# Kernel optimization log

Measured on AMD Instinct MI355X. Metric: run time of the kernel, lower is better.

## Reference

```python
import jax, jax.numpy as jnp
import numpy as np

# Static config (matches init_kwargs / chosen geometry)
DIM, HEADS, WS, SHIFT = 96, 3, 7, 3
H, W = 56, 56
B = 64
N = WS * WS
HID = int(DIM * 4.0)
EPS = 1e-5


def _rel_tables():
    # relative_coords_table: (1, 2*WS-1, 2*WS-1, 2), log-spaced coords in [-1,1]
    c = np.arange(-(WS - 1), WS, dtype=np.float32)
    tab = np.stack(np.meshgrid(c, c, indexing='ij'), axis=-1)[None]
    tab = tab / (WS - 1) * 8.0
    tab = np.sign(tab) * np.log2(np.abs(tab) + 1.0) / np.log2(8.0)
    # relative_position_index: (N, N) int
    coords = np.stack(np.meshgrid(np.arange(WS), np.arange(WS), indexing='ij'))
    cf = coords.reshape(2, -1)
    rel = (cf[:, :, None] - cf[:, None, :]).transpose(1, 2, 0).astype(np.int64)
    rel[..., 0] += WS - 1
    rel[..., 1] += WS - 1
    rel[..., 0] *= 2 * WS - 1
    return jnp.asarray(tab), jnp.asarray(rel.sum(-1))

_TABLE, _RPI = _rel_tables()


def _shift_mask():
    # standard SW-MSA mask: (num_windows, N, N), 0 / -100
    img = np.zeros((1, H, W, 1), dtype=np.float32)
    cnt = 0
    segs = (slice(0, -WS), slice(-WS, -SHIFT), slice(-SHIFT, None))
    for hs in segs:
        for ws_ in segs:
            img[:, hs, ws_, :] = cnt
            cnt += 1
    mw = img.reshape(1, H // WS, WS, W // WS, WS, 1).transpose(0, 1, 3, 2, 4, 5).reshape(-1, N)
    am = mw[:, None, :] - mw[:, :, None]
    return jnp.asarray(np.where(am != 0, -100.0, 0.0).astype(np.float32))


def _ln(x, g, b):
    mu = x.mean(-1, keepdims=True)
    var = x.var(-1, keepdims=True)
    return (x - mu) * jax.lax.rsqrt(var + EPS) * g + b


def setup_inputs() -> dict:
    key = jax.random.key(0)
    ks = jax.random.split(key, 8)
    s = 0.02
    return {
        'x': jax.random.normal(ks[0], (B, H * W, DIM), jnp.float32),
        'attn_mask': _shift_mask(),
        'qkv_w': jax.random.normal(ks[1], (3 * DIM, DIM), jnp.float32) * s,
        'q_bias': jnp.zeros((DIM,), jnp.float32),
        'v_bias': jnp.zeros((DIM,), jnp.float32),
        'logit_scale': jnp.full((HEADS, 1, 1), np.log(10.0), jnp.float32),
        'cpb_w1': jax.random.normal(ks[2], (512, 2), jnp.float32) * s,
        'cpb_b1': jnp.zeros((512,), jnp.float32),
        'cpb_w2': jax.random.normal(ks[3], (HEADS, 512), jnp.float32) * s,
        'proj_w': jax.random.normal(ks[4], (DIM, DIM), jnp.float32) * s,
        'proj_b': jnp.zeros((DIM,), jnp.float32),
        'norm1_g': jnp.ones((DIM,), jnp.float32),
        'norm1_b': jnp.zeros((DIM,), jnp.float32),
        'fc1_w': jax.random.normal(ks[5], (HID, DIM), jnp.float32) * s,
        'fc1_b': jnp.zeros((HID,), jnp.float32),
        'fc2_w': jax.random.normal(ks[6], (DIM, HID), jnp.float32) * s,
        'fc2_b': jnp.zeros((DIM,), jnp.float32),
        'norm2_g': jnp.ones((DIM,), jnp.float32),
        'norm2_b': jnp.zeros((DIM,), jnp.float32),
    }


def reference(x, attn_mask, qkv_w, q_bias, v_bias, logit_scale, cpb_w1, cpb_b1,
              cpb_w2, proj_w, proj_b, norm1_g, norm1_b, fc1_w, fc1_b, fc2_w,
              fc2_b, norm2_g, norm2_b):
    Bx, L, C = x.shape
    d = C // HEADS
    nH, nWd = H // WS, W // WS
    shortcut = x

    xi = x.reshape(Bx, H, W, C)
    xi = jnp.roll(xi, (-SHIFT, -SHIFT), axis=(1, 2))
    # window partition -> (Bx*nH*nWd, N, C)
    xw = xi.reshape(Bx, nH, WS, nWd, WS, C).transpose(0, 1, 3, 2, 4, 5).reshape(-1, N, C)

    # qkv with q/v bias only (k bias fixed to zero)
    qkv_bias = jnp.concatenate([q_bias, jnp.zeros_like(v_bias), v_bias])
    qkv = (xw @ qkv_w.T + qkv_bias).reshape(-1, N, 3, HEADS, d).transpose(2, 0, 3, 1, 4)
    q, k, v = qkv[0], qkv[1], qkv[2]  # (B_, h, N, d)

    # cosine attention with clamped learnable temperature
    qn = q / jnp.maximum(jnp.linalg.norm(q, axis=-1, keepdims=True), 1e-12)
    kn = k / jnp.maximum(jnp.linalg.norm(k, axis=-1, keepdims=True), 1e-12)
    attn = jnp.einsum('bhnd,bhmd->bhnm', qn, kn)
    scale = jnp.exp(jnp.minimum(logit_scale, jnp.log(jnp.float32(100.0))))
    attn = attn * scale

    # continuous relative position bias via cpb_mlp
    tab = jax.nn.gelu(_TABLE @ cpb_w1.T + cpb_b1, approximate=False) @ cpb_w2.T
    tab = tab.reshape(-1, HEADS)
    rpb = tab[_RPI.reshape(-1)].reshape(N, N, HEADS).transpose(2, 0, 1)
    attn = attn + (16.0 * jax.nn.sigmoid(rpb))[None]

    # shift mask
    nWin = attn_mask.shape[0]
    attn = attn.reshape(-1, nWin, HEADS, N, N) + attn_mask[None, :, None]
    attn = jax.nn.softmax(attn.reshape(-1, HEADS, N, N), axis=-1)

    out = jnp.einsum('bhnm,bhmd->bnhd', attn, v).reshape(-1, N, C)
    out = out @ proj_w.T + proj_b

    # window reverse + un-shift
    out = out.reshape(Bx, nH, nWd, WS, WS, C).transpose(0, 1, 3, 2, 4, 5).reshape(Bx, H, W, C)
    out = jnp.roll(out, (SHIFT, SHIFT), axis=(1, 2)).reshape(Bx, L, C)

    # SwinV2 post-norm residuals
    x1 = shortcut + _ln(out, norm1_g, norm1_b)
    h = jax.nn.gelu(x1 @ fc1_w.T + fc1_b, approximate=False) @ fc2_w.T + fc2_b
    return x1 + _ln(h, norm2_g, norm2_b)
```

## Files before the change

kernel.cpp:

```cpp
#include <hip/hip_runtime.h>
#include <math.h>

#define BATCH 64
#define HW 56
#define CDIM 96
#define NHEADS 3
#define WSZ 7
#define NTOK 49
#define SHIFT_ 3
#define NWIN_TOT 4096
#define HID 384
#define NTOKENS (BATCH * HW * HW)
#define LN100 4.6051702f

typedef __attribute__((ext_vector_type(8))) short bf16x8;
typedef __attribute__((ext_vector_type(8))) _Float16 f16x8;
typedef __attribute__((ext_vector_type(4))) float f32x4;

__device__ inline f32x4 mfma16(bf16x8 a, bf16x8 b, f32x4 c) {
  return __builtin_amdgcn_mfma_f32_16x16x32_bf16(a, b, c, 0, 0, 0);
}
__device__ inline f32x4 mfma16h(f16x8 a, f16x8 b, f32x4 c) {
  return __builtin_amdgcn_mfma_f32_16x16x32_f16(a, b, c, 0, 0, 0);
}

__device__ inline unsigned short f2b(float f) {
  unsigned u = __float_as_uint(f);
  unsigned r = (u + 0x7FFFu + ((u >> 16) & 1u)) >> 16;
  return (unsigned short)r;
}
__device__ inline float blo(unsigned u) { return __uint_as_float(u << 16); }
__device__ inline float bhi(unsigned u) { return __uint_as_float(u & 0xFFFF0000u); }
__device__ inline unsigned packb(float a, float b) {
  return (unsigned)f2b(a) | ((unsigned)f2b(b) << 16);
}
__device__ inline unsigned packh(float a, float b) {
  _Float16 ha = (_Float16)a, hb = (_Float16)b;
  unsigned short ua = *(unsigned short*)&ha, ub = *(unsigned short*)&hb;
  return (unsigned)ua | ((unsigned)ub << 16);
}
__device__ inline float gelu_f(float v) {
  float a = fabsf(v) * 0.70710678118654752f;
  float t = 1.0f / fmaf(a, 0.3275911f, 1.0f);
  float p = t * fmaf(t, fmaf(t, fmaf(t, fmaf(t, 1.061405429f, -1.453152027f),
                                     1.421413741f), -0.284496736f), 0.254829592f);
  float er = 1.0f - p * __expf(-a * a);
  er = (v < 0.f) ? -er : er;
  return 0.5f * v * (1.0f + er);
}

__global__ __launch_bounds__(256) void wconv2_kernel(
    const float* __restrict__ qkv_w, const float* __restrict__ fc1_w,
    const float* __restrict__ fc2_w, const float* __restrict__ proj_w,
    unsigned* __restrict__ qkvf, unsigned* __restrict__ w1f,
    unsigned* __restrict__ w2f, unsigned* __restrict__ pwf) {
  int T = blockIdx.x * 256 + threadIdx.x;
  if (T < 3456) {
    int tk = T >> 6, l = T & 63;
    int n = tk / 3, ks = tk - n * 3;
    int o = n * 16 + (l & 15);
    const float* src = qkv_w + o * 96 + ks * 32 + (l >> 4) * 8;
    uint4 d;
    d.x = packb(src[0], src[1]); d.y = packb(src[2], src[3]);
    d.z = packb(src[4], src[5]); d.w = packb(src[6], src[7]);
    *(uint4*)&qkvf[(size_t)(tk * 64 + l) * 4] = d;
    return;
  }
  T -= 3456;
  if (T < 4608) {
    int tk = T >> 6, l = T & 63;
    int n = tk / 3, ks = tk - n * 3;
    int o = n * 16 + (l & 15);
    const float* src = fc1_w + o * 96 + ks * 32 + (l >> 4) * 8;
    uint4 d;
    d.x = packb(src[0], src[1]); d.y = packb(src[2], src[3]);
    d.z = packb(src[4], src[5]); d.w = packb(src[6], src[7]);
    *(uint4*)&w1f[(size_t)(tk * 64 + l) * 4] = d;
    return;
  }
  T -= 4608;
  if (T < 4608) {
    int tk = T >> 6, l = T & 63;
    int n = tk / 12, ks = tk - n * 12;
    int o = n * 16 + (l & 15);
    const float* src = fc2_w + o * 384 + ks * 32 + (l >> 4) * 8;
    uint4 d;
    d.x = packb(src[0], src[1]); d.y = packb(src[2], src[3]);
    d.z = packb(src[4], src[5]); d.w = packb(src[6], src[7]);
    *(uint4*)&w2f[(size_t)(tk * 64 + l) * 4] = d;
    return;
  }
  T -= 4608;
  if (T < 1152) {
    int tk = T >> 6, l = T & 63;
    int n = tk / 3, ks = tk - n * 3;
    int o = n * 16 + (l & 15);
    const float* src = proj_w + o * 96 + ks * 32 + (l >> 4) * 8;
    uint4 d;
    d.x = packb(src[0], src[1]); d.y = packb(src[2], src[3]);
    d.z = packb(src[4], src[5]); d.w = packb(src[6], src[7]);
    *(uint4*)&pwf[(size_t)(tk * 64 + l) * 4] = d;
  }
}

__global__ __launch_bounds__(512) void cpb_table_kernel(
    const float* __restrict__ w1, const float* __restrict__ b1,
    const float* __restrict__ w2, float* __restrict__ tabout) {
  int tid = threadIdx.x;
  if (tid >= 169 * 3) return;
  int e = tid / 3, h = tid - e * 3;
  int i = e / 13, j = e - i * 13;
  float ti = (float)(i - 6) * (8.0f / 6.0f);
  float tj = (float)(j - 6) * (8.0f / 6.0f);
  float sx = (ti > 0.f) ? 1.f : (ti < 0.f ? -1.f : 0.f);
  float sy = (tj > 0.f) ? 1.f : (tj < 0.f ? -1.f : 0.f);
  float tx = sx * log2f(fabsf(ti) + 1.f) * (1.0f / 3.0f);
  float ty = sy * log2f(fabsf(tj) + 1.f) * (1.0f / 3.0f);
  float acc = 0.f;
  for (int jj = 0; jj < 512; ++jj) {
    float hv = tx * w1[jj * 2 + 0] + ty * w1[jj * 2 + 1] + b1[jj];
    float g = 0.5f * hv * (1.f + erff(hv * 0.70710678118654752f));
    acc += g * w2[h * 512 + jj];
  }
  tabout[e * 3 + h] = acc;
}

__global__ __launch_bounds__(256) void bm_kernel(
    const float* __restrict__ tabout, const float* __restrict__ mask,
    float* __restrict__ bmtab) {
  int idx = blockIdx.x * 256 + threadIdx.x;
  if (idx >= 64 * NHEADS * NTOK * NTOK) return;
  int wi = idx / (NHEADS * 2401);
  int rem = idx - wi * (NHEADS * 2401);
  int h = rem / 2401, ij = rem - h * 2401;
  int i = ij / NTOK, j = ij - i * NTOK;
  int ri = (i / WSZ) - (j / WSZ) + 6;
  int ci = (i % WSZ) - (j % WSZ) + 6;
  int e = ri * 13 + ci;
  float v = tabout[e * 3 + h];
  bmtab[idx] = 16.f / (1.f + expf(-v)) + mask[(size_t)wi * 2401 + ij];
}

__global__ __launch_bounds__(256) void qkv_mfma_kernel(
    const float* __restrict__ x, const unsigned* __restrict__ qkvf,
    const float* __restrict__ q_bias, const float* __restrict__ v_bias,
    const float* __restrict__ logit_scale,
    unsigned* __restrict__ qws, unsigned* __restrict__ kws,
    unsigned* __restrict__ vws) {
  __shared__ unsigned xa[64 * 52];
  int tid = threadIdx.x, lane = tid & 63, wv = tid >> 6;
  size_t tok0 = (size_t)blockIdx.x * 64;

  for (int idx = tid; idx < 3072; idx += 256) {
    int t = idx / 48, c2 = idx - t * 48;
    const float2 s = *(const float2*)(x + (tok0 + t) * 96 + c2 * 2);
    xa[t * 52 + c2] = packb(s.x, s.y);
  }
  __syncthreads();

  int c15 = lane & 15, q4 = lane >> 4;
  bf16x8 afr[3];
  #pragma unroll
  for (int k = 0; k < 3; ++k)
    afr[k] = *(const bf16x8*)&xa[(wv * 16 + c15) * 52 + k * 16 + q4 * 4];

  f32x4 acc[18];
  #pragma unroll
  for (int n = 0; n < 18; ++n) acc[n] = f32x4{0.f, 0.f, 0.f, 0.f};
  #pragma unroll
  for (int n = 0; n < 18; ++n) {
    #pragma unroll
    for (int k = 0; k < 3; ++k) {
      bf16x8 b = *(const bf16x8*)&qkvf[(size_t)((n * 3 + k) * 64 + lane) * 4];
      acc[n] = mfma16(afr[k], b, acc[n]);
    }
  }

  int tokr0 = (int)tok0 + wv * 16 + q4 * 4;
  int wbase[4];
  #pragma unroll
  for (int i = 0; i < 4; ++i) {
    int tk = tokr0 + i;
    int bb = tk / 3136, rem = tk - bb * 3136;
    int R = rem / 56, C = rem - R * 56;
    int rr = R + 53; if (rr >= 56) rr -= 56;
    int cc = C + 53; if (cc >= 56) cc -= 56;
    int wr = rr / 7, tr2 = rr - wr * 7;
    int wc = cc / 7, tc2 = cc - wc * 7;
    wbase[i] = (bb * 64 + wr * 8 + wc) * 2352 + (tr2 * 7 + tc2) * 16;
  }

  #pragma unroll
  for (int h = 0; h < 3; ++h) {
    float sc = expf(fminf(logit_scale[h], LN100));
    {
      f32x4 a0 = acc[2 * h], a1 = acc[2 * h + 1];
      float b0 = q_bias[h * 32 + c15], b1 = q_bias[h * 32 + 16 + c15];
      unsigned pk[8];
      #pragma unroll
      for (int i = 0; i < 4; ++i) {
        float va = a0[i] + b0, vb = a1[i] + b1;
        float ss = va * va + vb * vb;
        ss += __shfl_xor(ss, 1, 64); ss += __shfl_xor(ss, 2, 64);
        ss += __shfl_xor(ss, 4, 64); ss += __shfl_xor(ss, 8, 64);
        float inv = sc / fmaxf(sqrtf(ss), 1e-12f);
        va *= inv; vb *= inv;
        float pa = __shfl_xor(va, 1, 64), pb = __shfl_xor(vb, 1, 64);
        pk[i] = packb(va, pa); pk[4 + i] = packb(vb, pb);
      }
      if (!(lane & 1)) {
        int dw0 = c15 >> 1;
        #pragma unroll
        for (int i = 0; i < 4; ++i) {
          size_t base = (size_t)wbase[i] + h * 784;
          qws[base + dw0] = pk[i];
          qws[base + 8 + dw0] = pk[4 + i];
        }
      }
    }
    {
      f32x4 a0 = acc[6 + 2 * h], a1 = acc[7 + 2 * h];
      unsigned pk[8];
      #pragma unroll
      for (int i = 0; i < 4; ++i) {
        float va = a0[i], vb = a1[i];
        float ss = va * va + vb * vb;
        ss += __shfl_xor(ss, 1, 64); ss += __shfl_xor(ss, 2, 64);
        ss += __shfl_xor(ss, 4, 64); ss += __shfl_xor(ss, 8, 64);
        float inv = 1.f / fmaxf(sqrtf(ss), 1e-12f);
        va *= inv; vb *= inv;
        float pa = __shfl_xor(va, 1, 64), pb = __shfl_xor(vb, 1, 64);
        pk[i] = packb(va, pa); pk[4 + i] = packb(vb, pb);
      }
      if (!(lane & 1)) {
        int dw0 = c15 >> 1;
        #pragma unroll
        for (int i = 0; i < 4; ++i) {
          size_t base = (size_t)wbase[i] + h * 784;
          kws[base + dw0] = pk[i];
          kws[base + 8 + dw0] = pk[4 + i];
        }
      }
    }
    {
      f32x4 a0 = acc[12 + 2 * h], a1 = acc[13 + 2 * h];
      float b0 = v_bias[h * 32 + c15], b1 = v_bias[h * 32 + 16 + c15];
      unsigned pk[8];
      #pragma unroll
      for (int i = 0; i < 4; ++i) {
        float va = a0[i] + b0, vb = a1[i] + b1;
        float pa = __shfl_xor(va, 1, 64), pb = __shfl_xor(vb, 1, 64);
        pk[i] = packb(va, pa); pk[4 + i] = packb(vb, pb);
      }
      if (!(lane & 1)) {
        int dw0 = c15 >> 1;
        #pragma unroll
        for (int i = 0; i < 4; ++i) {
          size_t base = (size_t)wbase[i] + h * 784;
          vws[base + dw0] = pk[i];
          vws[base + 8 + dw0] = pk[4 + i];
        }
      }
    }
  }
}

__global__ __launch_bounds__(256) void attn_fused_kernel(
    const unsigned* __restrict__ qws, const unsigned* __restrict__ kws,
    const unsigned* __restrict__ vws, const float* __restrict__ bmtab,
    const unsigned* __restrict__ pwf, const float* __restrict__ proj_b,
    const float* __restrict__ x, const float* __restrict__ n1g,
    const float* __restrict__ n1b, float* __restrict__ out) {
  __shared__ __align__(16) unsigned smem[10368];
  _Float16* VtS  = (_Float16*)smem;
  unsigned* obuf = (unsigned*)smem;
  _Float16* Ph   = (_Float16*)((char*)smem + 13824);
  unsigned* Phd  = (unsigned*)((char*)smem + 13824);
  float*    ybuf = (float*)((char*)smem + 13824);

  int tid = threadIdx.x, lane = tid & 63, wv = tid >> 6;
  int c15 = lane & 15, q4 = lane >> 4;
  int win = blockIdx.x;
  int b = win >> 6, wi = win & 63, wh = wi >> 3, wcx = wi & 7;
  size_t wroot = (size_t)win * 2352;

  for (int idx = tid; idx < 768; idx += 256) {
    int h2 = idx >> 8, rem = idx & 255;
    int t = rem >> 2, dg = rem & 3;
    int tc2 = t > 48 ? 48 : t;
    uint4 v4 = *(const uint4*)&vws[wroot + h2 * 784 + tc2 * 16 + dg * 4];
    _Float16* dst = &VtS[h2 * 2304 + (dg * 8) * 72 + t];
    dst[0 * 72] = (_Float16)blo(v4.x); dst[1 * 72] = (_Float16)bhi(v4.x);
    dst[2 * 72] = (_Float16)blo(v4.y); dst[3 * 72] = (_Float16)bhi(v4.y);
    dst[4 * 72] = (_Float16)blo(v4.z); dst[5 * 72] = (_Float16)bhi(v4.z);
    dst[6 * 72] = (_Float16)blo(v4.w); dst[7 * 72] = (_Float16)bhi(v4.w);
  }
  __syncthreads();

  f32x4 oall[3][2];
  #pragma unroll
  for (int t = 0; t < 3; ++t)
    #pragma unroll
    for (int n2 = 0; n2 < 2; ++n2) oall[t][n2] = f32x4{0.f, 0.f, 0.f, 0.f};

  #pragma unroll
  for (int t = 0; t < 3; ++t) {
    int id = wv * 3 + t;
    int h = id >> 2, mm = id & 3;
    size_t wb = wroot + (size_t)h * 784;

    int tq = mm * 16 + c15; if (tq > 48) tq = 48;
    bf16x8 qf = *(const bf16x8*)&qws[wb + tq * 16 + q4 * 4];
    bf16x8 kf[4];
    #pragma unroll
    for (int n = 0; n < 4; ++n) {
      int tk = n * 16 + c15; if (tk > 48) tk = 48;
      kf[n] = *(const bf16x8*)&kws[wb + tk * 16 + q4 * 4];
    }

    f32x4 s[4];
    #pragma unroll
    for (int n = 0; n < 4; ++n)
      s[n] = mfma16(qf, kf[n], f32x4{0.f, 0.f, 0.f, 0.f});

    const float* bm = bmtab + ((size_t)wi * 3 + h) * 2401;
    #pragma unroll
    for (int i = 0; i < 4; ++i) {
      int rw = mm * 16 + 4 * q4 + i;
      if (rw < 49) {
        const float* br = bm + rw * 49;
        #pragma unroll
        for (int n = 0; n < 4; ++n) {
          int j = n * 16 + c15;
          s[n][i] = (j < 49) ? (s[n][i] + br[j]) : -1e30f;
        }
      } else {
        #pragma unroll
        for (int n = 0; n < 4; ++n)
          if (n * 16 + c15 >= 49) s[n][i] = -1e30f;
      }
    }

    #pragma unroll
    for (int i = 0; i < 4; ++i) {
      float mx = fmaxf(fmaxf(s[0][i], s[1][i]), fmaxf(s[2][i], s[3][i]));
      mx = fmaxf(mx, __shfl_xor(mx, 1, 64)); mx = fmaxf(mx, __shfl_xor(mx, 2, 64));
      mx = fmaxf(mx, __shfl_xor(mx, 4, 64)); mx = fmaxf(mx, __shfl_xor(mx, 8, 64));
      float sum = 0.f;
      #pragma unroll
      for (int n = 0; n < 4; ++n) { float e = __expf(s[n][i] - mx); s[n][i] = e; sum += e; }
      sum += __shfl_xor(sum, 1, 64); sum += __shfl_xor(sum, 2, 64);
      sum += __shfl_xor(sum, 4, 64); sum += __shfl_xor(sum, 8, 64);
      float inv = 1.f / sum;
      #pragma unroll
      for (int n = 0; n < 4; ++n) s[n][i] *= inv;
    }

    #pragma unroll
    for (int n = 0; n < 4; ++n)
      #pragma unroll
      for (int i = 0; i < 4; ++i) {
        float pv = s[n][i];
        float pn = __shfl_xor(pv, 1, 64);
        if (!(lane & 1)) {
          int row = mm * 16 + 4 * q4 + i;
          Phd[h * 2304 + row * 36 + n * 8 + (c15 >> 1)] = packh(pv, pn);
        }
      }
    asm volatile("s_waitcnt lgkmcnt(0)" ::: "memory");
    __builtin_amdgcn_sched_barrier(0);

    #pragma unroll
    for (int ks = 0; ks < 2; ++ks) {
      f16x8 pa = *(const f16x8*)&Ph[h * 4608 + (mm * 16 + c15) * 72 + ks * 32 + q4 * 8];
      #pragma unroll
      for (int n2 = 0; n2 < 2; ++n2) {
        f16x8 vb = *(const f16x8*)&VtS[h * 2304 + (n2 * 16 + c15) * 72 + ks * 32 + q4 * 8];
        oall[t][n2] = mfma16h(pa, vb, oall[t][n2]);
      }
    }
  }
  __syncthreads();

  #pragma unroll
  for (int t = 0; t < 3; ++t) {
    int id = wv * 3 + t;
    int h = id >> 2, mm = id & 3;
    #pragma unroll
    for (int n2 = 0; n2 < 2; ++n2)
      #pragma unroll
      for (int i = 0; i < 4; ++i) {
        float ov = oall[t][n2][i];
        float on = __shfl_xor(ov, 1, 64);
        if (!(lane & 1))
          obuf[(mm * 16 + 4 * q4 + i) * 52 + h * 16 + n2 * 8 + (c15 >> 1)] = packb(ov, on);
      }
  }
  __syncthreads();

  bf16x8 oa[3];
  #pragma unroll
  for (int ks = 0; ks < 3; ++ks)
    oa[ks] = *(const bf16x8*)&obuf[(wv * 16 + c15) * 52 + ks * 16 + q4 * 4];
  f32x4 pr[6];
  #pragma unroll
  for (int n = 0; n < 6; ++n) pr[n] = f32x4{0.f, 0.f, 0.f, 0.f};
  #pragma unroll
  for (int n = 0; n < 6; ++n)
    #pragma unroll
    for (int ks = 0; ks < 3; ++ks) {
      bf16x8 bfr = *(const bf16x8*)&pwf[(size_t)((n * 3 + ks) * 64 + lane) * 4];
      pr[n] = mfma16(oa[ks], bfr, pr[n]);
    }

  #pragma unroll
  for (int n = 0; n < 6; ++n) {
    int col = n * 16 + c15;
    float bo = proj_b[col];
    #pragma unroll
    for (int i = 0; i < 4; ++i)
      ybuf[(wv * 16 + 4 * q4 + i) * 100 + col] = pr[n][i] + bo;
  }
  __syncthreads();

  int t = tid >> 2, pp = tid & 3;
  if (t < 49) {
    const float* yrow = ybuf + t * 100 + pp * 24;
    float s1 = 0.f;
    #pragma unroll
    for (int c = 0; c < 24; ++c) s1 += yrow[c];
    s1 += __shfl_xor(s1, 1, 64); s1 += __shfl_xor(s1, 2, 64);
    float mu = s1 * (1.f / 96.f);
    float v2 = 0.f;
    #pragma unroll
    for (int c = 0; c < 24; ++c) { float d = yrow[c] - mu; v2 += d * d; }
    v2 += __shfl_xor(v2, 1, 64); v2 += __shfl_xor(v2, 2, 64);
    float rs = rsqrtf(v2 * (1.f / 96.f) + 1e-5f);
    int tr = (t * 9363) >> 16, tc = t - tr * 7;
    int R = wh * 7 + tr + SHIFT_; if (R >= HW) R -= HW;
    int C = wcx * 7 + tc + SHIFT_; if (C >= HW) C -= HW;
    size_t base = ((size_t)(b * 3136 + R * 56 + C)) * 96 + pp * 24;
    #pragma unroll
    for (int c4 = 0; c4 < 6; ++c4) {
      float4 xv = *(const float4*)(x + base + c4 * 4);
      float4 gv = *(const float4*)(n1g + pp * 24 + c4 * 4);
      float4 bv = *(const float4*)(n1b + pp * 24 + c4 * 4);
      float4 ov;
      ov.x = xv.x + (yrow[c4 * 4 + 0] - mu) * rs * gv.x + bv.x;
      ov.y = xv.y + (yrow[c4 * 4 + 1] - mu) * rs * gv.y + bv.y;
      ov.z = xv.z + (yrow[c4 * 4 + 2] - mu) * rs * gv.z + bv.z;
      ov.w = xv.w + (yrow[c4 * 4 + 3] - mu) * rs * gv.w + bv.w;
      *(float4*)(out + base + c4 * 4) = ov;
    }
  }
}

__global__ __launch_bounds__(256) void mlp_mfma_kernel(
    const unsigned* __restrict__ w1f, const float* __restrict__ fc1_b,
    const unsigned* __restrict__ w2f, const float* __restrict__ fc2_b,
    const float* __restrict__ n2g, const float* __restrict__ n2b,
    float* __restrict__ xio) {
  __shared__ unsigned xa[64 * 52];
  __shared__ unsigned hid[64 * 196];
  __shared__ float mu_s[64], rs_s[64];
  int tid = threadIdx.x, lane = tid & 63, wv = tid >> 6;
  int c15 = lane & 15, q4 = lane >> 4;
  size_t tok0 = (size_t)blockIdx.x * 64;

  for (int idx = tid; idx < 3072; idx += 256) {
    int t = idx / 48, c2 = idx - t * 48;
    const float2 s = *(const float2*)(xio + (tok0 + t) * 96 + c2 * 2);
    xa[t * 52 + c2] = packb(s.x, s.y);
  }
  __syncthreads();

  bf16x8 afr[4][3];
  #pragma unroll
  for (int m = 0; m < 4; ++m)
    #pragma unroll
    for (int k = 0; k < 3; ++k)
      afr[m][k] = *(const bf16x8*)&xa[(m * 16 + c15) * 52 + k * 16 + q4 * 4];
  f32x4 acc[4][6];
  #pragma unroll
  for (int m = 0; m < 4; ++m)
    #pragma unroll
    for (int n = 0; n < 6; ++n) acc[m][n] = f32x4{0.f, 0.f, 0.f, 0.f};
  #pragma unroll
  for (int n = 0; n < 6; ++n) {
    #pragma unroll
    for (int k = 0; k < 3; ++k) {
      bf16x8 b = *(const bf16x8*)&w1f[(size_t)(((6 * wv + n) * 3 + k) * 64 + lane) * 4];
      #pragma unroll
      for (int m = 0; m < 4; ++m) acc[m][n] = mfma16(afr[m][k], b, acc[m][n]);
    }
  }
  unsigned short* hidb = (unsigned short*)hid;
  #pragma unroll
  for (int n = 0; n < 6; ++n) {
    int col = (6 * wv + n) * 16 + c15;
    float bo = fc1_b[col];
    #pragma unroll
    for (int m = 0; m < 4; ++m) {
      #pragma unroll
      for (int i = 0; i < 4; ++i) {
        float g = gelu_f(acc[m][n][i] + bo);
        hidb[(m * 16 + q4 * 4 + i) * 392 + col] = f2b(g);
      }
    }
  }
  __syncthreads();

  f32x4 acc2[6];
  #pragma unroll
  for (int n = 0; n < 6; ++n) acc2[n] = f32x4{0.f, 0.f, 0.f, 0.f};
  #pragma unroll
  for (int k = 0; k < 12; ++k) {
    bf16x8 a = *(const bf16x8*)&hid[(wv * 16 + c15) * 196 + k * 16 + q4 * 4];
    #pragma unroll
    for (int n = 0; n < 6; ++n) {
      bf16x8 b = *(const bf16x8*)&w2f[(size_t)((n * 12 + k) * 64 + lane) * 4];
      acc2[n] = mfma16(a, b, acc2[n]);
    }
  }
  __syncthreads();

  float* ybuf = (float*)hid;
  #pragma unroll
  for (int n = 0; n < 6; ++n) {
    int col = n * 16 + c15;
    float bo = fc2_b[col];
    #pragma unroll
    for (int i = 0; i < 4; ++i)
      ybuf[(wv * 16 + q4 * 4 + i) * 100 + col] = acc2[n][i] + bo;
  }
  __syncthreads();

  {
    int t = tid >> 2, p = tid & 3;
    const float* row = ybuf + t * 100 + p * 24;
    float s = 0.f, s2 = 0.f;
    for (int c = 0; c < 24; ++c) { float v = row[c]; s += v; s2 += v * v; }
    s += __shfl_xor(s, 1, 64); s2 += __shfl_xor(s2, 1, 64);
    s += __shfl_xor(s, 2, 64); s2 += __shfl_xor(s2, 2, 64);
    if (p == 0) {
      float mu = s * (1.f / 96.f);
      float var = s2 * (1.f / 96.f) - mu * mu;
      mu_s[t] = mu;
      rs_s[t] = rsqrtf(fmaxf(var, 0.f) + 1e-5f);
    }
  }
  __syncthreads();

  for (int idx = tid; idx < 1536; idx += 256) {
    int t = idx / 24, c4 = (idx - t * 24) * 4;
    float mu = mu_s[t], rs = rs_s[t];
    float4 y4 = *(float4*)&ybuf[t * 100 + c4];
    float4 g4 = *(const float4*)&n2g[c4];
    float4 b4 = *(const float4*)&n2b[c4];
    float* gp = &xio[tok0 * 96 + t * 96 + c4];
    float4 x4 = *(const float4*)gp;
    float4 ov;
    ov.x = x4.x + (y4.x - mu) * rs * g4.x + b4.x;
    ov.y = x4.y + (y4.y - mu) * rs * g4.y + b4.y;
    ov.z = x4.z + (y4.z - mu) * rs * g4.z + b4.z;
    ov.w = x4.w + (y4.w - mu) * rs * g4.w + b4.w;
    *(float4*)gp = ov;
  }
}

extern "C" void kernel_launch(void* const* d_in, const int* in_sizes, int n_in,
                              void* d_out, int out_size, void* d_ws, size_t ws_size,
                              hipStream_t stream) {
  const float* x           = (const float*)d_in[0];
  const float* attn_mask   = (const float*)d_in[1];
  const float* qkv_w       = (const float*)d_in[2];
  const float* q_bias      = (const float*)d_in[3];
  const float* v_bias      = (const float*)d_in[4];
  const float* logit_scale = (const float*)d_in[5];
  const float* cpb_w1      = (const float*)d_in[6];
  const float* cpb_b1      = (const float*)d_in[7];
  const float* cpb_w2      = (const float*)d_in[8];
  const float* proj_w      = (const float*)d_in[9];
  const float* proj_b      = (const float*)d_in[10];
  const float* n1g         = (const float*)d_in[11];
  const float* n1b         = (const float*)d_in[12];
  const float* fc1_w       = (const float*)d_in[13];
  const float* fc1_b       = (const float*)d_in[14];
  const float* fc2_w       = (const float*)d_in[15];
  const float* fc2_b       = (const float*)d_in[16];
  const float* n2g         = (const float*)d_in[17];
  const float* n2b         = (const float*)d_in[18];
  float* out = (float*)d_out;

  float* tab     = (float*)d_ws;
  float* bmtab   = tab + 512;
  unsigned* qkvf = (unsigned*)(bmtab + 460992);
  unsigned* w1f  = qkvf + 13824;
  unsigned* w2f  = w1f + 18432;
  unsigned* pwf  = w2f + 18432;
  unsigned* qws  = pwf + 4608;
  unsigned* kws  = qws + 9633792;
  unsigned* vws  = kws + 9633792;

  wconv2_kernel<<<54, 256, 0, stream>>>(qkv_w, fc1_w, fc2_w, proj_w,
                                        qkvf, w1f, w2f, pwf);
  cpb_table_kernel<<<1, 512, 0, stream>>>(cpb_w1, cpb_b1, cpb_w2, tab);
  bm_kernel<<<(64 * NHEADS * NTOK * NTOK + 255) / 256, 256, 0, stream>>>(
      tab, attn_mask, bmtab);
  qkv_mfma_kernel<<<NTOKENS / 64, 256, 0, stream>>>(x, qkvf, q_bias, v_bias,
                                                    logit_scale, qws, kws, vws);
  attn_fused_kernel<<<NWIN_TOT, 256, 0, stream>>>(qws, kws, vws, bmtab,
                                                  pwf, proj_b, x, n1g, n1b, out);
  mlp_mfma_kernel<<<NTOKENS / 64, 256, 0, stream>>>(w1f, fc1_b, w2f, fc2_b,
                                                    n2g, n2b, out);
}
```

Baseline: 438.7 us.

## Emit bf16 copy of x1 from attention kernel and feed MLP directly

The attention epilogue now also writes a packed bf16 copy of the residual output x1 to a new workspace buffer. The MLP kernel loads its A fragments straight from that buffer in global memory, so the fp32 read, the conversion, the LDS staging and one barrier all go away. The hidden-layer store is also changed to pack two bf16 values per 32-bit write using a lane shuffle. This adds an extra write of about 38MB of bf16 in the attention kernel and needs more workspace. The fp32 x1 is still read later for the residual.

```diff
diff --git a/kernel.cpp b/kernel.cpp
--- a/kernel.cpp
+++ b/kernel.cpp
@@ -270,7 +270,8 @@
     const unsigned* __restrict__ vws, const float* __restrict__ bmtab,
     const unsigned* __restrict__ pwf, const float* __restrict__ proj_b,
     const float* __restrict__ x, const float* __restrict__ n1g,
-    const float* __restrict__ n1b, float* __restrict__ out) {
+    const float* __restrict__ n1b, float* __restrict__ out,
+    unsigned* __restrict__ x1bf) {
   __shared__ __align__(16) unsigned smem[10368];
   _Float16* VtS  = (_Float16*)smem;
   unsigned* obuf = (unsigned*)smem;
@@ -439,7 +440,9 @@
     int tr = (t * 9363) >> 16, tc = t - tr * 7;
     int R = wh * 7 + tr + SHIFT_; if (R >= HW) R -= HW;
     int C = wcx * 7 + tc + SHIFT_; if (C >= HW) C -= HW;
-    size_t base = ((size_t)(b * 3136 + R * 56 + C)) * 96 + pp * 24;
+    size_t tokorig = (size_t)(b * 3136 + R * 56 + C);
+    size_t base = tokorig * 96 + pp * 24;
+    unsigned bpk[12];
     #pragma unroll
     for (int c4 = 0; c4 < 6; ++c4) {
       float4 xv = *(const float4*)(x + base + c4 * 4);
@@ -451,7 +454,13 @@
       ov.z = xv.z + (yrow[c4 * 4 + 2] - mu) * rs * gv.z + bv.z;
       ov.w = xv.w + (yrow[c4 * 4 + 3] - mu) * rs * gv.w + bv.w;
       *(float4*)(out + base + c4 * 4) = ov;
-    }
+      bpk[c4 * 2 + 0] = packb(ov.x, ov.y);
+      bpk[c4 * 2 + 1] = packb(ov.z, ov.w);
+    }
+    unsigned* xb = x1bf + tokorig * 48 + pp * 12;
+    *(uint4*)&xb[0] = *(uint4*)&bpk[0];
+    *(uint4*)&xb[4] = *(uint4*)&bpk[4];
+    *(uint4*)&xb[8] = *(uint4*)&bpk[8];
   }
 }
 
@@ -459,27 +468,20 @@
     const unsigned* __restrict__ w1f, const float* __restrict__ fc1_b,
     const unsigned* __restrict__ w2f, const float* __restrict__ fc2_b,
     const float* __restrict__ n2g, const float* __restrict__ n2b,
-    float* __restrict__ xio) {
-  __shared__ unsigned xa[64 * 52];
+    const unsigned* __restrict__ x1bf, float* __restrict__ xio) {
   __shared__ unsigned hid[64 * 196];
   __shared__ float mu_s[64], rs_s[64];
   int tid = threadIdx.x, lane = tid & 63, wv = tid >> 6;
   int c15 = lane & 15, q4 = lane >> 4;
   size_t tok0 = (size_t)blockIdx.x * 64;
 
-  for (int idx = tid; idx < 3072; idx += 256) {
-    int t = idx / 48, c2 = idx - t * 48;
-    const float2 s = *(const float2*)(xio + (tok0 + t) * 96 + c2 * 2);
-    xa[t * 52 + c2] = packb(s.x, s.y);
-  }
-  __syncthreads();
-
   bf16x8 afr[4][3];
   #pragma unroll
   for (int m = 0; m < 4; ++m)
     #pragma unroll
     for (int k = 0; k < 3; ++k)
-      afr[m][k] = *(const bf16x8*)&xa[(m * 16 + c15) * 52 + k * 16 + q4 * 4];
+      afr[m][k] = *(const bf16x8*)&x1bf[(tok0 + m * 16 + c15) * 48 + k * 16 + q4 * 4];
+
   f32x4 acc[4][6];
   #pragma unroll
   for (int m = 0; m < 4; ++m)
@@ -494,7 +496,6 @@
       for (int m = 0; m < 4; ++m) acc[m][n] = mfma16(afr[m][k], b, acc[m][n]);
     }
   }
-  unsigned short* hidb = (unsigned short*)hid;
   #pragma unroll
   for (int n = 0; n < 6; ++n) {
     int col = (6 * wv + n) * 16 + c15;
@@ -504,7 +505,11 @@
       #pragma unroll
       for (int i = 0; i < 4; ++i) {
         float g = gelu_f(acc[m][n][i] + bo);
-        hidb[(m * 16 + q4 * 4 + i) * 392 + col] = f2b(g);
+        float gn = __shfl_xor(g, 1, 64);
+        if (!(lane & 1)) {
+          int row = m * 16 + q4 * 4 + i;
+          hid[row * 196 + (6 * wv + n) * 8 + (c15 >> 1)] = packb(g, gn);
+        }
       }
     }
   }
@@ -601,6 +606,7 @@
   unsigned* qws  = pwf + 4608;
   unsigned* kws  = qws + 9633792;
   unsigned* vws  = kws + 9633792;
+  unsigned* x1bf = vws + 9633792;
 
   wconv2_kernel<<<54, 256, 0, stream>>>(qkv_w, fc1_w, fc2_w, proj_w,
                                         qkvf, w1f, w2f, pwf);
@@ -610,7 +616,8 @@
   qkv_mfma_kernel<<<NTOKENS / 64, 256, 0, stream>>>(x, qkvf, q_bias, v_bias,
                                                     logit_scale, qws, kws, vws);
   attn_fused_kernel<<<NWIN_TOT, 256, 0, stream>>>(qws, kws, vws, bmtab,
-                                                  pwf, proj_b, x, n1g, n1b, out);
+                                                  pwf, proj_b, x, n1g, n1b, out,
+                                                  x1bf);
   mlp_mfma_kernel<<<NTOKENS / 64, 256, 0, stream>>>(w1f, fc1_b, w2f, fc2_b,
-                                                    n2g, n2b, out);
-}
+                                                    n2g, n2b, x1bf, out);
+}
```

After: 531.8 us. +21.2%, slower.

## Fuse MLP into attention kernel per window, keeping x1 in shared memory

Applied to the files above, without the earlier changes.

Merges the MLP kernel into the windowed attention kernel. Each block now holds its window's 49 post-attention tokens (x1) in shared memory and runs fc1, GELU, fc2 and LayerNorm2 on them directly. This removes the global write and re-read of the intermediate activation tensor and one kernel launch. In exchange the block's shared memory grows to about 76KB, which may lower occupancy, and the MLP now processes 49-token tiles padded to 64, wasting MFMA work on the padding rows.

```diff
diff --git a/kernel.cpp b/kernel.cpp
--- a/kernel.cpp
+++ b/kernel.cpp
@@ -38,6 +38,11 @@
   _Float16 ha = (_Float16)a, hb = (_Float16)b;
   unsigned short ua = *(unsigned short*)&ha, ub = *(unsigned short*)&hb;
   return (unsigned)ua | ((unsigned)ub << 16);
+}
+__device__ inline bf16x8 mk8(unsigned d0, unsigned d1, unsigned d2, unsigned d3) {
+  union { unsigned u[4]; bf16x8 v; } c;
+  c.u[0] = d0; c.u[1] = d1; c.u[2] = d2; c.u[3] = d3;
+  return c.v;
 }
 __device__ inline float gelu_f(float v) {
   float a = fabsf(v) * 0.70710678118654752f;
@@ -265,18 +270,25 @@
   }
 }
 
-__global__ __launch_bounds__(256) void attn_fused_kernel(
+__global__ __launch_bounds__(256) void attn_mlp_fused_kernel(
     const unsigned* __restrict__ qws, const unsigned* __restrict__ kws,
     const unsigned* __restrict__ vws, const float* __restrict__ bmtab,
     const unsigned* __restrict__ pwf, const float* __restrict__ proj_b,
     const float* __restrict__ x, const float* __restrict__ n1g,
-    const float* __restrict__ n1b, float* __restrict__ out) {
-  __shared__ __align__(16) unsigned smem[10368];
-  _Float16* VtS  = (_Float16*)smem;
-  unsigned* obuf = (unsigned*)smem;
-  _Float16* Ph   = (_Float16*)((char*)smem + 13824);
-  unsigned* Phd  = (unsigned*)((char*)smem + 13824);
-  float*    ybuf = (float*)((char*)smem + 13824);
+    const float* __restrict__ n1b, const unsigned* __restrict__ w1f,
+    const float* __restrict__ fc1_b, const unsigned* __restrict__ w2f,
+    const float* __restrict__ fc2_b, const float* __restrict__ n2g,
+    const float* __restrict__ n2b, float* __restrict__ out) {
+  __shared__ __align__(16) unsigned smem[19072];
+  _Float16* VtS   = (_Float16*)smem;
+  _Float16* Ph    = (_Float16*)((char*)smem + 13824);
+  unsigned* Phd   = (unsigned*)((char*)smem + 13824);
+  float*    ybuf  = (float*)smem;
+  unsigned* obuf  = (unsigned*)((char*)smem + 25600);
+  unsigned* hid   = (unsigned*)((char*)smem + 25600);
+  float*    ybuf2 = (float*)((char*)smem + 25600);
+  float*    mu_s  = (float*)((char*)smem + 75776);
+  float*    rs_s  = (float*)((char*)smem + 76032);
 
   int tid = threadIdx.x, lane = tid & 63, wv = tid >> 6;
   int c15 = lane & 15, q4 = lane >> 4;
@@ -412,7 +424,6 @@
       bf16x8 bfr = *(const bf16x8*)&pwf[(size_t)((n * 3 + ks) * 64 + lane) * 4];
       pr[n] = mfma16(oa[ks], bfr, pr[n]);
     }
-
   #pragma unroll
   for (int n = 0; n < 6; ++n) {
     int col = n * 16 + c15;
@@ -423,54 +434,37 @@
   }
   __syncthreads();
 
-  int t = tid >> 2, pp = tid & 3;
-  if (t < 49) {
-    const float* yrow = ybuf + t * 100 + pp * 24;
-    float s1 = 0.f;
-    #pragma unroll
-    for (int c = 0; c < 24; ++c) s1 += yrow[c];
-    s1 += __shfl_xor(s1, 1, 64); s1 += __shfl_xor(s1, 2, 64);
-    float mu = s1 * (1.f / 96.f);
-    float v2 = 0.f;
-    #pragma unroll
-    for (int c = 0; c < 24; ++c) { float d = yrow[c] - mu; v2 += d * d; }
-    v2 += __shfl_xor(v2, 1, 64); v2 += __shfl_xor(v2, 2, 64);
-    float rs = rsqrtf(v2 * (1.f / 96.f) + 1e-5f);
-    int tr = (t * 9363) >> 16, tc = t - tr * 7;
-    int R = wh * 7 + tr + SHIFT_; if (R >= HW) R -= HW;
-    int C = wcx * 7 + tc + SHIFT_; if (C >= HW) C -= HW;
-    size_t base = ((size_t)(b * 3136 + R * 56 + C)) * 96 + pp * 24;
-    #pragma unroll
-    for (int c4 = 0; c4 < 6; ++c4) {
-      float4 xv = *(const float4*)(x + base + c4 * 4);
-      float4 gv = *(const float4*)(n1g + pp * 24 + c4 * 4);
-      float4 bv = *(const float4*)(n1b + pp * 24 + c4 * 4);
-      float4 ov;
-      ov.x = xv.x + (yrow[c4 * 4 + 0] - mu) * rs * gv.x + bv.x;
-      ov.y = xv.y + (yrow[c4 * 4 + 1] - mu) * rs * gv.y + bv.y;
-      ov.z = xv.z + (yrow[c4 * 4 + 2] - mu) * rs * gv.z + bv.z;
-      ov.w = xv.w + (yrow[c4 * 4 + 3] - mu) * rs * gv.w + bv.w;
-      *(float4*)(out + base + c4 * 4) = ov;
-    }
-  }
-}
-
-__global__ __launch_bounds__(256) void mlp_mfma_kernel(
-    const unsigned* __restrict__ w1f, const float* __restrict__ fc1_b,
-    const unsigned* __restrict__ w2f, const float* __restrict__ fc2_b,
-    const float* __restrict__ n2g, const float* __restrict__ n2b,
-    float* __restrict__ xio) {
-  __shared__ unsigned xa[64 * 52];
-  __shared__ unsigned hid[64 * 196];
-  __shared__ float mu_s[64], rs_s[64];
-  int tid = threadIdx.x, lane = tid & 63, wv = tid >> 6;
-  int c15 = lane & 15, q4 = lane >> 4;
-  size_t tok0 = (size_t)blockIdx.x * 64;
-
-  for (int idx = tid; idx < 3072; idx += 256) {
-    int t = idx / 48, c2 = idx - t * 48;
-    const float2 s = *(const float2*)(xio + (tok0 + t) * 96 + c2 * 2);
-    xa[t * 52 + c2] = packb(s.x, s.y);
+  {
+    int t = tid >> 2, pp = tid & 3;
+    if (t < 49) {
+      float* yrow = ybuf + t * 100 + pp * 24;
+      float s1 = 0.f;
+      #pragma unroll
+      for (int c = 0; c < 24; ++c) s1 += yrow[c];
+      s1 += __shfl_xor(s1, 1, 64); s1 += __shfl_xor(s1, 2, 64);
+      float mu = s1 * (1.f / 96.f);
+      float v2 = 0.f;
+      #pragma unroll
+      for (int c = 0; c < 24; ++c) { float d = yrow[c] - mu; v2 += d * d; }
+      v2 += __shfl_xor(v2, 1, 64); v2 += __shfl_xor(v2, 2, 64);
+      float rs = rsqrtf(v2 * (1.f / 96.f) + 1e-5f);
+      int tr = (t * 9363) >> 16, tc = t - tr * 7;
+      int R = wh * 7 + tr + SHIFT_; if (R >= HW) R -= HW;
+      int C = wcx * 7 + tc + SHIFT_; if (C >= HW) C -= HW;
+      size_t base = ((size_t)(b * 3136 + R * 56 + C)) * 96 + pp * 24;
+      #pragma unroll
+      for (int c4 = 0; c4 < 6; ++c4) {
+        float4 xv = *(const float4*)(x + base + c4 * 4);
+        float4 gv = *(const float4*)(n1g + pp * 24 + c4 * 4);
+        float4 bv = *(const float4*)(n1b + pp * 24 + c4 * 4);
+        float4 ov;
+        ov.x = xv.x + (yrow[c4 * 4 + 0] - mu) * rs * gv.x + bv.x;
+        ov.y = xv.y + (yrow[c4 * 4 + 1] - mu) * rs * gv.y + bv.y;
+        ov.z = xv.z + (yrow[c4 * 4 + 2] - mu) * rs * gv.z + bv.z;
+        ov.w = xv.w + (yrow[c4 * 4 + 3] - mu) * rs * gv.w + bv.w;
+        *(float4*)&yrow[c4 * 4] = ov;
+      }
+    }
   }
   __syncthreads();
 
@@ -478,8 +472,13 @@
   #pragma unroll
   for (int m = 0; m < 4; ++m)
     #pragma unroll
-    for (int k = 0; k < 3; ++k)
-      afr[m][k] = *(const bf16x8*)&xa[(m * 16 + c15) * 52 + k * 16 + q4 * 4];
+    for (int k = 0; k < 3; ++k) {
+      const float* src = &ybuf[(m * 16 + c15) * 100 + k * 32 + q4 * 8];
+      float4 a0 = *(const float4*)&src[0];
+      float4 a1 = *(const float4*)&src[4];
+      afr[m][k] = mk8(packb(a0.x, a0.y), packb(a0.z, a0.w),
+                      packb(a1.x, a1.y), packb(a1.z, a1.w));
+    }
   f32x4 acc[4][6];
   #pragma unroll
   for (int m = 0; m < 4; ++m)
@@ -489,22 +488,24 @@
   for (int n = 0; n < 6; ++n) {
     #pragma unroll
     for (int k = 0; k < 3; ++k) {
-      bf16x8 b = *(const bf16x8*)&w1f[(size_t)(((6 * wv + n) * 3 + k) * 64 + lane) * 4];
-      #pragma unroll
-      for (int m = 0; m < 4; ++m) acc[m][n] = mfma16(afr[m][k], b, acc[m][n]);
-    }
-  }
-  unsigned short* hidb = (unsigned short*)hid;
-  #pragma unroll
-  for (int n = 0; n < 6; ++n) {
-    int col = (6 * wv + n) * 16 + c15;
-    float bo = fc1_b[col];
-    #pragma unroll
-    for (int m = 0; m < 4; ++m) {
-      #pragma unroll
-      for (int i = 0; i < 4; ++i) {
-        float g = gelu_f(acc[m][n][i] + bo);
-        hidb[(m * 16 + q4 * 4 + i) * 392 + col] = f2b(g);
+      bf16x8 bb = *(const bf16x8*)&w1f[(size_t)(((6 * wv + n) * 3 + k) * 64 + lane) * 4];
+      #pragma unroll
+      for (int m = 0; m < 4; ++m) acc[m][n] = mfma16(afr[m][k], bb, acc[m][n]);
+    }
+  }
+  {
+    unsigned short* hidb = (unsigned short*)hid;
+    #pragma unroll
+    for (int n = 0; n < 6; ++n) {
+      int col = (6 * wv + n) * 16 + c15;
+      float bo = fc1_b[col];
+      #pragma unroll
+      for (int m = 0; m < 4; ++m) {
+        #pragma unroll
+        for (int i = 0; i < 4; ++i) {
+          float g = gelu_f(acc[m][n][i] + bo);
+          hidb[(m * 16 + q4 * 4 + i) * 392 + col] = f2b(g);
+        }
       }
     }
   }
@@ -518,26 +519,25 @@
     bf16x8 a = *(const bf16x8*)&hid[(wv * 16 + c15) * 196 + k * 16 + q4 * 4];
     #pragma unroll
     for (int n = 0; n < 6; ++n) {
-      bf16x8 b = *(const bf16x8*)&w2f[(size_t)((n * 12 + k) * 64 + lane) * 4];
-      acc2[n] = mfma16(a, b, acc2[n]);
-    }
-  }
-  __syncthreads();
-
-  float* ybuf = (float*)hid;
+      bf16x8 bb = *(const bf16x8*)&w2f[(size_t)((n * 12 + k) * 64 + lane) * 4];
+      acc2[n] = mfma16(a, bb, acc2[n]);
+    }
+  }
+  __syncthreads();
+
   #pragma unroll
   for (int n = 0; n < 6; ++n) {
     int col = n * 16 + c15;
     float bo = fc2_b[col];
     #pragma unroll
     for (int i = 0; i < 4; ++i)
-      ybuf[(wv * 16 + q4 * 4 + i) * 100 + col] = acc2[n][i] + bo;
+      ybuf2[(wv * 16 + q4 * 4 + i) * 100 + col] = acc2[n][i] + bo;
   }
   __syncthreads();
 
   {
     int t = tid >> 2, p = tid & 3;
-    const float* row = ybuf + t * 100 + p * 24;
+    const float* row = ybuf2 + t * 100 + p * 24;
     float s = 0.f, s2 = 0.f;
     for (int c = 0; c < 24; ++c) { float v = row[c]; s += v; s2 += v * v; }
     s += __shfl_xor(s, 1, 64); s2 += __shfl_xor(s2, 1, 64);
@@ -551,20 +551,28 @@
   }
   __syncthreads();
 
-  for (int idx = tid; idx < 1536; idx += 256) {
-    int t = idx / 24, c4 = (idx - t * 24) * 4;
-    float mu = mu_s[t], rs = rs_s[t];
-    float4 y4 = *(float4*)&ybuf[t * 100 + c4];
-    float4 g4 = *(const float4*)&n2g[c4];
-    float4 b4 = *(const float4*)&n2b[c4];
-    float* gp = &xio[tok0 * 96 + t * 96 + c4];
-    float4 x4 = *(const float4*)gp;
-    float4 ov;
-    ov.x = x4.x + (y4.x - mu) * rs * g4.x + b4.x;
-    ov.y = x4.y + (y4.y - mu) * rs * g4.y + b4.y;
-    ov.z = x4.z + (y4.z - mu) * rs * g4.z + b4.z;
-    ov.w = x4.w + (y4.w - mu) * rs * g4.w + b4.w;
-    *(float4*)gp = ov;
+  {
+    int t = tid >> 2, pp = tid & 3;
+    if (t < 49) {
+      float mu = mu_s[t], rs = rs_s[t];
+      int tr = (t * 9363) >> 16, tc = t - tr * 7;
+      int R = wh * 7 + tr + SHIFT_; if (R >= HW) R -= HW;
+      int C = wcx * 7 + tc + SHIFT_; if (C >= HW) C -= HW;
+      size_t base = ((size_t)(b * 3136 + R * 56 + C)) * 96 + pp * 24;
+      #pragma unroll
+      for (int c4 = 0; c4 < 6; ++c4) {
+        float4 x1v = *(float4*)&ybuf[t * 100 + pp * 24 + c4 * 4];
+        float4 h4  = *(float4*)&ybuf2[t * 100 + pp * 24 + c4 * 4];
+        float4 g4  = *(const float4*)&n2g[pp * 24 + c4 * 4];
+        float4 b4  = *(const float4*)&n2b[pp * 24 + c4 * 4];
+        float4 ov;
+        ov.x = x1v.x + (h4.x - mu) * rs * g4.x + b4.x;
+        ov.y = x1v.y + (h4.y - mu) * rs * g4.y + b4.y;
+        ov.z = x1v.z + (h4.z - mu) * rs * g4.z + b4.z;
+        ov.w = x1v.w + (h4.w - mu) * rs * g4.w + b4.w;
+        *(float4*)(out + base + c4 * 4) = ov;
+      }
+    }
   }
 }
 
@@ -609,8 +617,7 @@
       tab, attn_mask, bmtab);
   qkv_mfma_kernel<<<NTOKENS / 64, 256, 0, stream>>>(x, qkvf, q_bias, v_bias,
                                                     logit_scale, qws, kws, vws);
-  attn_fused_kernel<<<NWIN_TOT, 256, 0, stream>>>(qws, kws, vws, bmtab,
-                                                  pwf, proj_b, x, n1g, n1b, out);
-  mlp_mfma_kernel<<<NTOKENS / 64, 256, 0, stream>>>(w1f, fc1_b, w2f, fc2_b,
-                                                    n2g, n2b, out);
-}
+  attn_mlp_fused_kernel<<<NWIN_TOT, 256, 0, stream>>>(
+      qws, kws, vws, bmtab, pwf, proj_b, x, n1g, n1b,
+      w1f, fc1_b, w2f, fc2_b, n2g, n2b, out);
+}
```

Result: slower. 454.0 us (+3.5%).
